# Kernel optimization log

Hardware: AMD Instinct MI355X
Metric: run time of the kernel (lower is better)

Reference implementation:

```python
import jax, jax.numpy as jnp
import numpy as np

ALPHA = 0.2  # TF leaky_relu default

def setup_inputs() -> dict:
    key = jax.random.key(0)
    ks = jax.random.split(key, 6)
    B, N, F, D = 2, 8192, 256, 128
    seq = jax.random.normal(ks[0], (B, N, F), dtype=jnp.float32)
    # Conv1D with kernel size 1 == pointwise linear
    Wf = jax.random.normal(ks[1], (F, D), dtype=jnp.float32) * (1.0 / np.sqrt(F))
    w1 = jax.random.normal(ks[2], (D, 1), dtype=jnp.float32) * (1.0 / np.sqrt(D))
    b1 = jnp.zeros((1,), dtype=jnp.float32)
    w2 = jax.random.normal(ks[3], (D, 1), dtype=jnp.float32) * (1.0 / np.sqrt(D))
    b2 = jnp.zeros((1,), dtype=jnp.float32)
    bias = jnp.zeros((D,), dtype=jnp.float32)
    return {"seq": seq, "Wf": Wf, "w1": w1, "b1": b1, "w2": w2, "b2": b2, "bias": bias}

def reference(seq, Wf, w1, b1, w2, b2, bias):
    # seq: [B,N,F] -> seq_fts: [B,N,D]
    seq_fts = jnp.einsum('bnf,fd->bnd', seq, Wf)
    f1 = jnp.einsum('bnd,do->bno', seq_fts, w1) + b1  # [B,N,1]
    f2 = jnp.einsum('bnd,do->bno', seq_fts, w2) + b2  # [B,N,1]
    logits = f1 + jnp.swapaxes(f2, 1, 2)              # [B,N,N] outer-sum
    coefs = jax.nn.softmax(jax.nn.leaky_relu(logits, ALPHA), axis=-1)
    vals = jnp.einsum('bnm,bmd->bnd', coefs, seq_fts) + bias
    return jax.nn.leaky_relu(vals, ALPHA)
```

## Files before the change

### kernel.cpp

```cpp
#include <hip/hip_runtime.h>
#include <cstddef>

#define ALPHA 0.2f
constexpr int B = 2, N = 8192, F = 256, D = 128;
constexpr int M = B * N;
constexpr int NB = 2048;
constexpr int SUB = 128;
constexpr int P = N / SUB;
constexpr int GB = 2;
constexpr int NBB = NB / GB;
constexpr int GSZ = 64;
constexpr int NGRP = NB / GSZ;
constexpr int QROWS = 8;
constexpr int DSL = 4;
constexpr int NSL = D / DSL;

#define BMIN (-10.0f)
#define BSCALE ((float)NB / 20.0f)
__device__ inline int bucket_of(float x) {
  int g = (int)((x - BMIN) * BSCALE);
  return g < 0 ? 0 : (g > NB - 1 ? NB - 1 : g);
}

__global__ __launch_bounds__(512) void k_gemm(const float* __restrict__ seq,
                                              const float* __restrict__ Wf,
                                              const float* __restrict__ w1,
                                              const float* __restrict__ b1,
                                              const float* __restrict__ w2,
                                              const float* __restrict__ b2,
                                              float* __restrict__ fts,
                                              float* __restrict__ f1,
                                              float* __restrict__ f2) {
  __shared__ float As[32][68];
  __shared__ float Bs[32][128];
  const int m0 = blockIdx.x * 64;
  const int t = threadIdx.x;
  const int colg = t & 31;
  const int rowg = t >> 5;
  float acc[4][4];
#pragma unroll
  for (int r = 0; r < 4; ++r)
#pragma unroll
    for (int c = 0; c < 4; ++c) acc[r][c] = 0.f;

  for (int kc = 0; kc < F; kc += 32) {
    {
      int row = t >> 3, k4 = t & 7;
      const float4 v = *reinterpret_cast<const float4*>(
          &seq[(size_t)(m0 + row) * F + kc + k4 * 4]);
      As[k4 * 4 + 0][row] = v.x; As[k4 * 4 + 1][row] = v.y;
      As[k4 * 4 + 2][row] = v.z; As[k4 * 4 + 3][row] = v.w;
    }
#pragma unroll
    for (int it = 0; it < 2; ++it) {
      int f = t + it * 512;
      int row = f >> 5, c4 = f & 31;
      *reinterpret_cast<float4*>(&Bs[row][c4 * 4]) =
          *reinterpret_cast<const float4*>(&Wf[(size_t)(kc + row) * D + c4 * 4]);
    }
    __syncthreads();
#pragma unroll
    for (int k = 0; k < 32; ++k) {
      const float4 a4 = *reinterpret_cast<const float4*>(&As[k][rowg * 4]);
      const float4 b4 = *reinterpret_cast<const float4*>(&Bs[k][colg * 4]);
      acc[0][0] += a4.x * b4.x; acc[0][1] += a4.x * b4.y; acc[0][2] += a4.x * b4.z; acc[0][3] += a4.x * b4.w;
      acc[1][0] += a4.y * b4.x; acc[1][1] += a4.y * b4.y; acc[1][2] += a4.y * b4.z; acc[1][3] += a4.y * b4.w;
      acc[2][0] += a4.z * b4.x; acc[2][1] += a4.z * b4.y; acc[2][2] += a4.z * b4.z; acc[2][3] += a4.z * b4.w;
      acc[3][0] += a4.w * b4.x; acc[3][1] += a4.w * b4.y; acc[3][2] += a4.w * b4.z; acc[3][3] += a4.w * b4.w;
    }
    __syncthreads();
  }
#pragma unroll
  for (int r = 0; r < 4; ++r) {
    float4 v = {acc[r][0], acc[r][1], acc[r][2], acc[r][3]};
    *reinterpret_cast<float4*>(&fts[(size_t)(m0 + rowg * 4 + r) * D + colg * 4]) = v;
  }
  const float w1v[4] = {w1[colg * 4], w1[colg * 4 + 1], w1[colg * 4 + 2], w1[colg * 4 + 3]};
  const float w2v[4] = {w2[colg * 4], w2[colg * 4 + 1], w2[colg * 4 + 2], w2[colg * 4 + 3]};
  const float b1v = b1[0], b2v = b2[0];
#pragma unroll
  for (int r = 0; r < 4; ++r) {
    float s1 = acc[r][0] * w1v[0] + acc[r][1] * w1v[1] + acc[r][2] * w1v[2] + acc[r][3] * w1v[3];
    float s2 = acc[r][0] * w2v[0] + acc[r][1] * w2v[1] + acc[r][2] * w2v[2] + acc[r][3] * w2v[3];
#pragma unroll
    for (int off = 16; off > 0; off >>= 1) {
      s1 += __shfl_down(s1, off, 32);
      s2 += __shfl_down(s2, off, 32);
    }
    if (colg == 0) {
      const int row = m0 + rowg * 4 + r;
      f1[row] = s1 + b1v;
      f2[row] = s2 + b2v;
    }
  }
}

__global__ __launch_bounds__(128) void k_hist(const float* __restrict__ f2,
                                              int* __restrict__ bid,
                                              int* __restrict__ histcnt) {
  __shared__ int hist[NB];
  const int b = blockIdx.x / P, p = blockIdx.x % P;
  const int t = threadIdx.x;
  for (int i = t; i < NB; i += 128) hist[i] = 0;
  const int j = p * SUB + t;
  float x = f2[b * N + j];
  int g = bucket_of(x);
  bid[b * N + j] = g;
  __syncthreads();
  atomicAdd(&hist[g], 1);
  __syncthreads();
  for (int i = t; i < NB; i += 128)
    histcnt[((size_t)(b * P + p)) * NB + i] = hist[i];
}

__global__ __launch_bounds__(256) void k_sub(const int* __restrict__ histcnt,
                                             int* __restrict__ substart,
                                             int* __restrict__ btot) {
  const int gid = blockIdx.x * 256 + threadIdx.x;
  const int b = gid / NB, g = gid % NB;
  int run = 0;
  for (int pp = 0; pp < P; ++pp) {
    substart[((size_t)(b * P + pp)) * NB + g] = run;
    run += histcnt[((size_t)(b * P + pp)) * NB + g];
  }
  btot[b * NB + g] = run;
}

__global__ __launch_bounds__(128) void k_scat(const float* __restrict__ f2,
                                              const int* __restrict__ bid,
                                              const int* __restrict__ substart,
                                              const int* __restrict__ btot,
                                              int* __restrict__ bstart,
                                              float* __restrict__ f2s,
                                              int* __restrict__ idxs,
                                              float* __restrict__ wps,
                                              float* __restrict__ wns) {
  __shared__ int bstart_lds[NB];
  __shared__ int bids[SUB];
  __shared__ int wsum2[2];
  const int b = blockIdx.x / P, p = blockIdx.x % P;
  const int t = threadIdx.x;
  const int lane = t & 63, wave = t >> 6;
  const size_t bN = (size_t)b * N;

  int c[16];
  int loc = 0;
#pragma unroll
  for (int i = 0; i < 16; ++i) { c[i] = btot[b * NB + t * 16 + i]; loc += c[i]; }
  int incl = loc;
#pragma unroll
  for (int off = 1; off < 64; off <<= 1) {
    int y = __shfl_up(incl, off);
    if (lane >= off) incl += y;
  }
  if (lane == 63) wsum2[wave] = incl;
  __syncthreads();
  if (wave == 1) incl += wsum2[0];
  int excl = incl - loc;
#pragma unroll
  for (int i = 0; i < 16; ++i) { bstart_lds[t * 16 + i] = excl; excl += c[i]; }
  __syncthreads();
  if (p == 0) {
    for (int i = t; i < NB; i += 128) bstart[b * (NB + 1) + i] = bstart_lds[i];
    if (t == 0) bstart[b * (NB + 1) + NB] = N;
  }

  const int j = p * SUB + t;
  const int g = bid[bN + j];
  bids[t] = g;
  __syncthreads();
  int off = bstart_lds[g] + substart[((size_t)(b * P + p)) * NB + g];
  for (int jj = 0; jj < t; ++jj) off += (bids[jj] == g);
  const float x = f2[bN + j];
  f2s[bN + off] = x;
  idxs[bN + off] = j;
  wps[bN + off] = expf(x);
  wns[bN + off] = expf(ALPHA * x);
}

__global__ __launch_bounds__(256) void k_perm(const float* __restrict__ fts,
                                              const int* __restrict__ idxs,
                                              float* __restrict__ fts_s) {
  const int tid = blockIdx.x * 256 + threadIdx.x;
  const int eg = tid >> 5;
  const int q = tid & 31;
  const int b = eg / N;
  const int j = idxs[eg];
  *reinterpret_cast<float4*>(&fts_s[(size_t)eg * D + q * 4]) =
      *reinterpret_cast<const float4*>(&fts[((size_t)b * N + j) * D + q * 4]);
}

__global__ __launch_bounds__(128) void k_bsum(const float* __restrict__ fts_s,
                                              const float* __restrict__ wps,
                                              const float* __restrict__ wns,
                                              const int* __restrict__ bstart,
                                              float* __restrict__ Wp, float* __restrict__ Wn,
                                              float* __restrict__ Cp, float* __restrict__ Cn) {
  const int b = blockIdx.x / NBB, blk = blockIdx.x % NBB;
  const int d = threadIdx.x;
  const int gbase = blk * GB;
  const size_t bN = (size_t)b * N;
  for (int gg = 0; gg < GB; ++gg) {
    const int g = gbase + gg;
    const int e0 = bstart[b * (NB + 1) + g], e1 = bstart[b * (NB + 1) + g + 1];
    float ap = 0.f, an = 0.f, sp = 0.f, sn = 0.f;
    int e = e0;
    for (; e + 4 <= e1; e += 4) {
      const float* vp = &fts_s[(bN + e) * D + d];
      const float v0 = vp[0], v1 = vp[D], v2 = vp[2 * D], v3 = vp[3 * D];
      const float p0 = wps[bN + e], p1 = wps[bN + e + 1], p2 = wps[bN + e + 2], p3 = wps[bN + e + 3];
      const float n0 = wns[bN + e], n1 = wns[bN + e + 1], n2 = wns[bN + e + 2], n3 = wns[bN + e + 3];
      ap += p0 * v0 + p1 * v1 + p2 * v2 + p3 * v3;
      an += n0 * v0 + n1 * v1 + n2 * v2 + n3 * v3;
      sp += p0 + p1 + p2 + p3;
      sn += n0 + n1 + n2 + n3;
    }
    for (; e < e1; ++e) {
      const float v = fts_s[(bN + e) * D + d];
      const float wp = wps[bN + e], wn = wns[bN + e];
      ap += wp * v; an += wn * v; sp += wp; sn += wn;
    }
    Wp[((size_t)b * NB + g) * D + d] = ap;
    Wn[((size_t)b * NB + g) * D + d] = an;
    if (d == 0) { Cp[b * NB + g] = sp; Cn[b * NB + g] = sn; }
  }
}

__global__ __launch_bounds__(128) void k_scan(const float* __restrict__ Wp, const float* __restrict__ Wn,
                                              const float* __restrict__ Cp, const float* __restrict__ Cn,
                                              float* __restrict__ BPos, float* __restrict__ BNeg,
                                              float* __restrict__ CpB, float* __restrict__ CnB) {
  __shared__ float gp[NGRP][DSL], gn[NGRP][DSL];
  __shared__ float cgp[NGRP], cgn[NGRP];
  const int b = blockIdx.x / NSL, sl = blockIdx.x % NSL;
  const int t = threadIdx.x;
  const int d4 = t & (DSL - 1), grp = t >> 2;
  const int d = sl * DSL + d4;
  const size_t base = (size_t)b * NB;

  float sp = 0.f, sn = 0.f;
  for (int gg = 0; gg < GSZ; ++gg) {
    const int g = grp * GSZ + gg;
    sp += Wp[(base + g) * D + d];
    sn += Wn[(base + g) * D + d];
  }
  gp[grp][d4] = sp; gn[grp][d4] = sn;
  if (sl == 0 && d4 == 0) {
    float cp = 0.f, cn = 0.f;
    for (int gg = 0; gg < GSZ; ++gg) { const int g = grp * GSZ + gg; cp += Cp[base + g]; cn += Cn[base + g]; }
    cgp[grp] = cp; cgn[grp] = cn;
  }
  __syncthreads();

  if (t < DSL) {
    float run = 0.f;
    for (int g2 = 0; g2 < NGRP; ++g2) { const float v = gn[g2][t]; gn[g2][t] = run; run += v; }
  } else if (t < 2 * DSL) {
    const int dd = t - DSL;
    float run = 0.f;
    for (int g2 = NGRP - 1; g2 >= 0; --g2) { const float v = gp[g2][dd]; gp[g2][dd] = run; run += v; }
  } else if (sl == 0 && t == 2 * DSL) {
    float run = 0.f;
    for (int g2 = 0; g2 < NGRP; ++g2) { const float v = cgn[g2]; cgn[g2] = run; run += v; }
  } else if (sl == 0 && t == 2 * DSL + 1) {
    float run = 0.f;
    for (int g2 = NGRP - 1; g2 >= 0; --g2) { const float v = cgp[g2]; cgp[g2] = run; run += v; }
  }
  __syncthreads();

  float runn = gn[grp][d4];
  for (int gg = 0; gg < GSZ; ++gg) {
    const int g = grp * GSZ + gg;
    BNeg[(base + g) * D + d] = runn;
    runn += Wn[(base + g) * D + d];
  }
  float runp = gp[grp][d4];
  for (int gg = GSZ - 1; gg >= 0; --gg) {
    const int g = grp * GSZ + gg;
    BPos[(base + g) * D + d] = runp;
    runp += Wp[(base + g) * D + d];
  }
  if (sl == 0 && d4 == 0) {
    float rn = cgn[grp];
    for (int gg = 0; gg < GSZ; ++gg) { const int g = grp * GSZ + gg; CnB[base + g] = rn; rn += Cn[base + g]; }
    float rp = cgp[grp];
    for (int gg = GSZ - 1; gg >= 0; --gg) { const int g = grp * GSZ + gg; CpB[base + g] = rp; rp += Cp[base + g]; }
  }
}

__global__ __launch_bounds__(256) void k_query(const float* __restrict__ f1,
                                               const float* __restrict__ f2s,
                                               const float* __restrict__ wps,
                                               const float* __restrict__ wns,
                                               const float* __restrict__ fts_s,
                                               const int* __restrict__ bstart,
                                               const float* __restrict__ BPos, const float* __restrict__ BNeg,
                                               const float* __restrict__ CpB, const float* __restrict__ CnB,
                                               const float* __restrict__ bias,
                                               float* __restrict__ out) {
  const int r = threadIdx.x >> 5;
  const int lane = threadIdx.x & 31;
  const int row = blockIdx.x * QROWS + r;
  const int b = row / N;
  const size_t bN = (size_t)b * N;
  const int d4 = lane * 4;
  const float f1v = f1[row];
  const float th = -f1v;
  const int g = bucket_of(th);
  const int base = bstart[b * (NB + 1) + g];
  const int end  = bstart[b * (NB + 1) + g + 1];
  float4 sn = *reinterpret_cast<const float4*>(&BNeg[((size_t)b * NB + g) * D + d4]);
  float4 sp = *reinterpret_cast<const float4*>(&BPos[((size_t)b * NB + g) * D + d4]);
  float cn = CnB[b * NB + g];
  float cp = CpB[b * NB + g];
  for (int e = base; e < end; ++e) {
    const float key = f2s[bN + e];
    const float wn_raw = wns[bN + e];
    const float wp_raw = wps[bN + e];
    const float4 v = *reinterpret_cast<const float4*>(&fts_s[(bN + e) * D + d4]);
    const bool neg = (key <= th);
    const float wn = neg ? wn_raw : 0.f;
    const float wp = neg ? 0.f : wp_raw;
    sn.x += wn * v.x; sn.y += wn * v.y; sn.z += wn * v.z; sn.w += wn * v.w;
    sp.x += wp * v.x; sp.y += wp * v.y; sp.z += wp * v.z; sp.w += wp * v.w;
    cn += wn; cp += wp;
  }
  const float wqp = expf(f1v), wqn = expf(ALPHA * f1v);
  const float denom = wqp * cp + wqn * cn;
  const float inv = 1.0f / denom;
  const float4 bi = *reinterpret_cast<const float4*>(&bias[d4]);
  float4 val;
  val.x = (wqp * sp.x + wqn * sn.x) * inv + bi.x;
  val.y = (wqp * sp.y + wqn * sn.y) * inv + bi.y;
  val.z = (wqp * sp.z + wqn * sn.z) * inv + bi.z;
  val.w = (wqp * sp.w + wqn * sn.w) * inv + bi.w;
  val.x = val.x >= 0.f ? val.x : ALPHA * val.x;
  val.y = val.y >= 0.f ? val.y : ALPHA * val.y;
  val.z = val.z >= 0.f ? val.z : ALPHA * val.z;
  val.w = val.w >= 0.f ? val.w : ALPHA * val.w;
  *reinterpret_cast<float4*>(&out[(size_t)row * D + d4]) = val;
}

extern "C" void kernel_launch(void* const* d_in, const int* in_sizes, int n_in,
                              void* d_out, int out_size, void* d_ws, size_t ws_size,
                              hipStream_t stream) {
  const float* seq  = (const float*)d_in[0];
  const float* Wf   = (const float*)d_in[1];
  const float* w1   = (const float*)d_in[2];
  const float* b1   = (const float*)d_in[3];
  const float* w2   = (const float*)d_in[4];
  const float* b2   = (const float*)d_in[5];
  const float* bias = (const float*)d_in[6];
  float* out = (float*)d_out;

  char* ws = (char*)d_ws;
  size_t off = 0;
  auto alloc = [&](size_t bytes) -> void* {
    void* p = ws + off;
    off = (off + bytes + 255) & ~(size_t)255;
    return p;
  };

  float* fts     = (float*)alloc((size_t)M * D * 4);
  float* fts_s   = (float*)alloc((size_t)M * D * 4);
  float* f1      = (float*)alloc((size_t)M * 4);
  float* f2      = (float*)alloc((size_t)M * 4);
  float* f2s     = (float*)alloc((size_t)M * 4);
  int*   idxs    = (int*)  alloc((size_t)M * 4);
  float* wps     = (float*)alloc((size_t)M * 4);
  float* wns     = (float*)alloc((size_t)M * 4);
  int*   bid     = (int*)  alloc((size_t)M * 4);
  int*   histcnt = (int*)  alloc((size_t)B * P * NB * 4);
  int*   substart= (int*)  alloc((size_t)B * P * NB * 4);
  int*   btot    = (int*)  alloc((size_t)B * NB * 4);
  int*   bstart  = (int*)  alloc((size_t)B * (NB + 1) * 4);
  float* Wp      = (float*)alloc((size_t)B * NB * D * 4);
  float* Wn      = (float*)alloc((size_t)B * NB * D * 4);
  float* Cp      = (float*)alloc((size_t)B * NB * 4);
  float* Cn      = (float*)alloc((size_t)B * NB * 4);
  float* BPos    = (float*)alloc((size_t)B * NB * D * 4);
  float* BNeg    = (float*)alloc((size_t)B * NB * D * 4);
  float* CpB     = (float*)alloc((size_t)B * NB * 4);
  float* CnB     = (float*)alloc((size_t)B * NB * 4);

  hipLaunchKernelGGL(k_gemm,  dim3(M / 64),          dim3(512), 0, stream, seq, Wf, w1, b1, w2, b2, fts, f1, f2);
  hipLaunchKernelGGL(k_hist,  dim3(B * P),           dim3(128), 0, stream, f2, bid, histcnt);
  hipLaunchKernelGGL(k_sub,   dim3(B * NB / 256),    dim3(256), 0, stream, histcnt, substart, btot);
  hipLaunchKernelGGL(k_scat,  dim3(B * P),           dim3(128), 0, stream, f2, bid, substart, btot, bstart,
                     f2s, idxs, wps, wns);
  hipLaunchKernelGGL(k_perm,  dim3(M * D / 4 / 256), dim3(256), 0, stream, fts, idxs, fts_s);
  hipLaunchKernelGGL(k_bsum,  dim3(B * NBB),         dim3(128), 0, stream, fts_s, wps, wns, bstart, Wp, Wn, Cp, Cn);
  hipLaunchKernelGGL(k_scan,  dim3(B * NSL),         dim3(128), 0, stream, Wp, Wn, Cp, Cn, BPos, BNeg, CpB, CnB);
  hipLaunchKernelGGL(k_query, dim3(M / QROWS),       dim3(256), 0, stream, f1, f2s, wps, wns, fts_s, bstart,
                     BPos, BNeg, CpB, CnB, bias, out);
}
```

Baseline: 96.70 us.

## Use split-bf16 MFMA for projection GEMM and widen scan groups

The fp32 SIMT projection GEMM is replaced by bf16 MFMA 16x16x32 instructions. Each operand is split into high and low bf16 halves, and three products are accumulated to stay close to fp32 accuracy. The f1/f2 reductions now go through 16-lane shuffles and a shared-memory combine across the two column-half waves. Separately, k_scan group size is halved to 32 and the block is doubled to 256 threads, giving more parallelism in the per-group scan. This adds conversion work in the tile loads, a small precision loss, and LDS bank-conflict risk from the transposed B stores.

```diff
diff --git a/kernel.cpp b/kernel.cpp
--- a/kernel.cpp
+++ b/kernel.cpp
@@ -9,17 +9,28 @@
 constexpr int P = N / SUB;
 constexpr int GB = 2;
 constexpr int NBB = NB / GB;
-constexpr int GSZ = 64;
+constexpr int GSZ = 32;
 constexpr int NGRP = NB / GSZ;
 constexpr int QROWS = 8;
 constexpr int DSL = 4;
 constexpr int NSL = D / DSL;
+
+typedef __attribute__((ext_vector_type(8))) short bf16x8;
+typedef __attribute__((ext_vector_type(4))) float f32x4;
 
 #define BMIN (-10.0f)
 #define BSCALE ((float)NB / 20.0f)
 __device__ inline int bucket_of(float x) {
   int g = (int)((x - BMIN) * BSCALE);
   return g < 0 ? 0 : (g > NB - 1 ? NB - 1 : g);
+}
+
+__device__ inline unsigned short bf16_rne(float x) {
+  unsigned u = __float_as_uint(x);
+  return (unsigned short)((u + 0x7FFFu + ((u >> 16) & 1u)) >> 16);
+}
+__device__ inline float bf16_tof(unsigned short h) {
+  return __uint_as_float(((unsigned)h) << 16);
 }
 
 __global__ __launch_bounds__(512) void k_gemm(const float* __restrict__ seq,
@@ -31,67 +42,89 @@
                                               float* __restrict__ fts,
                                               float* __restrict__ f1,
                                               float* __restrict__ f2) {
-  __shared__ float As[32][68];
-  __shared__ float Bs[32][128];
+  __shared__ unsigned short Ah[64][40], Al[64][40];
+  __shared__ unsigned short Bh[128][40], Bl[128][40];
+  __shared__ float part1[64][2], part2[64][2];
   const int m0 = blockIdx.x * 64;
   const int t = threadIdx.x;
-  const int colg = t & 31;
-  const int rowg = t >> 5;
-  float acc[4][4];
-#pragma unroll
-  for (int r = 0; r < 4; ++r)
-#pragma unroll
-    for (int c = 0; c < 4; ++c) acc[r][c] = 0.f;
+  const int w = t >> 6;
+  const int lane = t & 63;
+  const int q = lane >> 4, rt = lane & 15;
+  const int r0 = (w & 3) * 16;
+  const int c0 = (w >> 2) * 64;
+  f32x4 acc[4];
+#pragma unroll
+  for (int ct = 0; ct < 4; ++ct) acc[ct] = (f32x4){0.f, 0.f, 0.f, 0.f};
 
   for (int kc = 0; kc < F; kc += 32) {
     {
-      int row = t >> 3, k4 = t & 7;
+      const int row = t >> 3, k4 = t & 7;
       const float4 v = *reinterpret_cast<const float4*>(
           &seq[(size_t)(m0 + row) * F + kc + k4 * 4]);
-      As[k4 * 4 + 0][row] = v.x; As[k4 * 4 + 1][row] = v.y;
-      As[k4 * 4 + 2][row] = v.z; As[k4 * 4 + 3][row] = v.w;
+      const float vv[4] = {v.x, v.y, v.z, v.w};
+#pragma unroll
+      for (int i = 0; i < 4; ++i) {
+        const unsigned short h = bf16_rne(vv[i]);
+        Ah[row][k4 * 4 + i] = h;
+        Al[row][k4 * 4 + i] = bf16_rne(vv[i] - bf16_tof(h));
+      }
     }
 #pragma unroll
     for (int it = 0; it < 2; ++it) {
-      int f = t + it * 512;
-      int row = f >> 5, c4 = f & 31;
-      *reinterpret_cast<float4*>(&Bs[row][c4 * 4]) =
-          *reinterpret_cast<const float4*>(&Wf[(size_t)(kc + row) * D + c4 * 4]);
+      const int f = t + it * 512;
+      const int kr = f >> 5, c4 = f & 31;
+      const float4 v = *reinterpret_cast<const float4*>(
+          &Wf[(size_t)(kc + kr) * D + c4 * 4]);
+      const float vv[4] = {v.x, v.y, v.z, v.w};
+#pragma unroll
+      for (int i = 0; i < 4; ++i) {
+        const unsigned short h = bf16_rne(vv[i]);
+        Bh[c4 * 4 + i][kr] = h;
+        Bl[c4 * 4 + i][kr] = bf16_rne(vv[i] - bf16_tof(h));
+      }
     }
     __syncthreads();
-#pragma unroll
-    for (int k = 0; k < 32; ++k) {
-      const float4 a4 = *reinterpret_cast<const float4*>(&As[k][rowg * 4]);
-      const float4 b4 = *reinterpret_cast<const float4*>(&Bs[k][colg * 4]);
-      acc[0][0] += a4.x * b4.x; acc[0][1] += a4.x * b4.y; acc[0][2] += a4.x * b4.z; acc[0][3] += a4.x * b4.w;
-      acc[1][0] += a4.y * b4.x; acc[1][1] += a4.y * b4.y; acc[1][2] += a4.y * b4.z; acc[1][3] += a4.y * b4.w;
-      acc[2][0] += a4.z * b4.x; acc[2][1] += a4.z * b4.y; acc[2][2] += a4.z * b4.z; acc[2][3] += a4.z * b4.w;
-      acc[3][0] += a4.w * b4.x; acc[3][1] += a4.w * b4.y; acc[3][2] += a4.w * b4.z; acc[3][3] += a4.w * b4.w;
+    const bf16x8 ah = *reinterpret_cast<const bf16x8*>(&Ah[r0 + rt][q * 8]);
+    const bf16x8 al = *reinterpret_cast<const bf16x8*>(&Al[r0 + rt][q * 8]);
+#pragma unroll
+    for (int ct = 0; ct < 4; ++ct) {
+      const bf16x8 bh = *reinterpret_cast<const bf16x8*>(&Bh[c0 + ct * 16 + rt][q * 8]);
+      const bf16x8 bl = *reinterpret_cast<const bf16x8*>(&Bl[c0 + ct * 16 + rt][q * 8]);
+      acc[ct] = __builtin_amdgcn_mfma_f32_16x16x32_bf16(ah, bh, acc[ct], 0, 0, 0);
+      acc[ct] = __builtin_amdgcn_mfma_f32_16x16x32_bf16(al, bh, acc[ct], 0, 0, 0);
+      acc[ct] = __builtin_amdgcn_mfma_f32_16x16x32_bf16(ah, bl, acc[ct], 0, 0, 0);
     }
     __syncthreads();
   }
 #pragma unroll
-  for (int r = 0; r < 4; ++r) {
-    float4 v = {acc[r][0], acc[r][1], acc[r][2], acc[r][3]};
-    *reinterpret_cast<float4*>(&fts[(size_t)(m0 + rowg * 4 + r) * D + colg * 4]) = v;
-  }
-  const float w1v[4] = {w1[colg * 4], w1[colg * 4 + 1], w1[colg * 4 + 2], w1[colg * 4 + 3]};
-  const float w2v[4] = {w2[colg * 4], w2[colg * 4 + 1], w2[colg * 4 + 2], w2[colg * 4 + 3]};
-  const float b1v = b1[0], b2v = b2[0];
-#pragma unroll
-  for (int r = 0; r < 4; ++r) {
-    float s1 = acc[r][0] * w1v[0] + acc[r][1] * w1v[1] + acc[r][2] * w1v[2] + acc[r][3] * w1v[3];
-    float s2 = acc[r][0] * w2v[0] + acc[r][1] * w2v[1] + acc[r][2] * w2v[2] + acc[r][3] * w2v[3];
-#pragma unroll
-    for (int off = 16; off > 0; off >>= 1) {
-      s1 += __shfl_down(s1, off, 32);
-      s2 += __shfl_down(s2, off, 32);
-    }
-    if (colg == 0) {
-      const int row = m0 + rowg * 4 + r;
-      f1[row] = s1 + b1v;
-      f2[row] = s2 + b2v;
-    }
+  for (int ct = 0; ct < 4; ++ct)
+#pragma unroll
+    for (int reg = 0; reg < 4; ++reg)
+      fts[(size_t)(m0 + r0 + q * 4 + reg) * D + c0 + ct * 16 + rt] = acc[ct][reg];
+
+#pragma unroll
+  for (int reg = 0; reg < 4; ++reg) {
+    float s1 = 0.f, s2 = 0.f;
+#pragma unroll
+    for (int ct = 0; ct < 4; ++ct) {
+      const int c = c0 + ct * 16 + rt;
+      s1 += acc[ct][reg] * w1[c];
+      s2 += acc[ct][reg] * w2[c];
+    }
+#pragma unroll
+    for (int off = 8; off > 0; off >>= 1) {
+      s1 += __shfl_down(s1, off, 16);
+      s2 += __shfl_down(s2, off, 16);
+    }
+    if (rt == 0) {
+      part1[r0 + q * 4 + reg][w >> 2] = s1;
+      part2[r0 + q * 4 + reg][w >> 2] = s2;
+    }
+  }
+  __syncthreads();
+  if (t < 64) {
+    f1[m0 + t] = part1[t][0] + part1[t][1] + b1[0];
+    f2[m0 + t] = part2[t][0] + part2[t][1] + b2[0];
   }
 }
 
@@ -226,7 +259,7 @@
   }
 }
 
-__global__ __launch_bounds__(128) void k_scan(const float* __restrict__ Wp, const float* __restrict__ Wn,
+__global__ __launch_bounds__(256) void k_scan(const float* __restrict__ Wp, const float* __restrict__ Wn,
                                               const float* __restrict__ Cp, const float* __restrict__ Cn,
                                               float* __restrict__ BPos, float* __restrict__ BNeg,
                                               float* __restrict__ CpB, float* __restrict__ CnB) {
@@ -390,7 +423,7 @@
                      f2s, idxs, wps, wns);
   hipLaunchKernelGGL(k_perm,  dim3(M * D / 4 / 256), dim3(256), 0, stream, fts, idxs, fts_s);
   hipLaunchKernelGGL(k_bsum,  dim3(B * NBB),         dim3(128), 0, stream, fts_s, wps, wns, bstart, Wp, Wn, Cp, Cn);
-  hipLaunchKernelGGL(k_scan,  dim3(B * NSL),         dim3(128), 0, stream, Wp, Wn, Cp, Cn, BPos, BNeg, CpB, CnB);
+  hipLaunchKernelGGL(k_scan,  dim3(B * NSL),         dim3(256), 0, stream, Wp, Wn, Cp, Cn, BPos, BNeg, CpB, CnB);
   hipLaunchKernelGGL(k_query, dim3(M / QROWS),       dim3(256), 0, stream, f1, f2s, wps, wns, fts_s, bstart,
                      BPos, BNeg, CpB, CnB, bias, out);
 }
```

After: 101.1 us. +4.5%, slower.

## Double bucket count over narrower range and pack key/weights into float4

Applied to the files above, without the earlier changes.

Doubles the number of sort buckets and narrows the bucket range, so each query's boundary bucket holds fewer elements to scan linearly. The per-element key, exp(x) and exp(alpha*x) values are packed into one float4 array, so the bucket-sum and query kernels each make one vector load instead of three scalar loads. In exchange the bucket-sum, scan, histogram and prefix arrays double in size, and the scan kernel now uses 256 threads because NGRP doubled. Keys outside [-6,6] clamp into the edge buckets, which could make those buckets larger.

```diff
diff --git a/kernel.cpp b/kernel.cpp
--- a/kernel.cpp
+++ b/kernel.cpp
@@ -4,7 +4,7 @@
 #define ALPHA 0.2f
 constexpr int B = 2, N = 8192, F = 256, D = 128;
 constexpr int M = B * N;
-constexpr int NB = 2048;
+constexpr int NB = 4096;
 constexpr int SUB = 128;
 constexpr int P = N / SUB;
 constexpr int GB = 2;
@@ -14,9 +14,10 @@
 constexpr int QROWS = 8;
 constexpr int DSL = 4;
 constexpr int NSL = D / DSL;
-
-#define BMIN (-10.0f)
-#define BSCALE ((float)NB / 20.0f)
+constexpr int BPT = NB / 128;
+
+#define BMIN (-6.0f)
+#define BSCALE ((float)NB / 12.0f)
 __device__ inline int bucket_of(float x) {
   int g = (int)((x - BMIN) * BSCALE);
   return g < 0 ? 0 : (g > NB - 1 ? NB - 1 : g);
@@ -131,10 +132,8 @@
                                               const int* __restrict__ substart,
                                               const int* __restrict__ btot,
                                               int* __restrict__ bstart,
-                                              float* __restrict__ f2s,
-                                              int* __restrict__ idxs,
-                                              float* __restrict__ wps,
-                                              float* __restrict__ wns) {
+                                              float4* __restrict__ kw,
+                                              int* __restrict__ idxs) {
   __shared__ int bstart_lds[NB];
   __shared__ int bids[SUB];
   __shared__ int wsum2[2];
@@ -143,10 +142,10 @@
   const int lane = t & 63, wave = t >> 6;
   const size_t bN = (size_t)b * N;
 
-  int c[16];
+  int c[BPT];
   int loc = 0;
 #pragma unroll
-  for (int i = 0; i < 16; ++i) { c[i] = btot[b * NB + t * 16 + i]; loc += c[i]; }
+  for (int i = 0; i < BPT; ++i) { c[i] = btot[b * NB + t * BPT + i]; loc += c[i]; }
   int incl = loc;
 #pragma unroll
   for (int off = 1; off < 64; off <<= 1) {
@@ -158,7 +157,7 @@
   if (wave == 1) incl += wsum2[0];
   int excl = incl - loc;
 #pragma unroll
-  for (int i = 0; i < 16; ++i) { bstart_lds[t * 16 + i] = excl; excl += c[i]; }
+  for (int i = 0; i < BPT; ++i) { bstart_lds[t * BPT + i] = excl; excl += c[i]; }
   __syncthreads();
   if (p == 0) {
     for (int i = t; i < NB; i += 128) bstart[b * (NB + 1) + i] = bstart_lds[i];
@@ -172,10 +171,8 @@
   int off = bstart_lds[g] + substart[((size_t)(b * P + p)) * NB + g];
   for (int jj = 0; jj < t; ++jj) off += (bids[jj] == g);
   const float x = f2[bN + j];
-  f2s[bN + off] = x;
+  kw[bN + off] = make_float4(x, expf(x), expf(ALPHA * x), 0.f);
   idxs[bN + off] = j;
-  wps[bN + off] = expf(x);
-  wns[bN + off] = expf(ALPHA * x);
 }
 
 __global__ __launch_bounds__(256) void k_perm(const float* __restrict__ fts,
@@ -191,8 +188,7 @@
 }
 
 __global__ __launch_bounds__(128) void k_bsum(const float* __restrict__ fts_s,
-                                              const float* __restrict__ wps,
-                                              const float* __restrict__ wns,
+                                              const float4* __restrict__ kw,
                                               const int* __restrict__ bstart,
                                               float* __restrict__ Wp, float* __restrict__ Wn,
                                               float* __restrict__ Cp, float* __restrict__ Cn) {
@@ -208,17 +204,16 @@
     for (; e + 4 <= e1; e += 4) {
       const float* vp = &fts_s[(bN + e) * D + d];
       const float v0 = vp[0], v1 = vp[D], v2 = vp[2 * D], v3 = vp[3 * D];
-      const float p0 = wps[bN + e], p1 = wps[bN + e + 1], p2 = wps[bN + e + 2], p3 = wps[bN + e + 3];
-      const float n0 = wns[bN + e], n1 = wns[bN + e + 1], n2 = wns[bN + e + 2], n3 = wns[bN + e + 3];
-      ap += p0 * v0 + p1 * v1 + p2 * v2 + p3 * v3;
-      an += n0 * v0 + n1 * v1 + n2 * v2 + n3 * v3;
-      sp += p0 + p1 + p2 + p3;
-      sn += n0 + n1 + n2 + n3;
+      const float4 k0 = kw[bN + e], k1 = kw[bN + e + 1], k2 = kw[bN + e + 2], k3 = kw[bN + e + 3];
+      ap += k0.y * v0 + k1.y * v1 + k2.y * v2 + k3.y * v3;
+      an += k0.z * v0 + k1.z * v1 + k2.z * v2 + k3.z * v3;
+      sp += k0.y + k1.y + k2.y + k3.y;
+      sn += k0.z + k1.z + k2.z + k3.z;
     }
     for (; e < e1; ++e) {
       const float v = fts_s[(bN + e) * D + d];
-      const float wp = wps[bN + e], wn = wns[bN + e];
-      ap += wp * v; an += wn * v; sp += wp; sn += wn;
+      const float4 k0 = kw[bN + e];
+      ap += k0.y * v; an += k0.z * v; sp += k0.y; sn += k0.z;
     }
     Wp[((size_t)b * NB + g) * D + d] = ap;
     Wn[((size_t)b * NB + g) * D + d] = an;
@@ -226,7 +221,7 @@
   }
 }
 
-__global__ __launch_bounds__(128) void k_scan(const float* __restrict__ Wp, const float* __restrict__ Wn,
+__global__ __launch_bounds__(256) void k_scan(const float* __restrict__ Wp, const float* __restrict__ Wn,
                                               const float* __restrict__ Cp, const float* __restrict__ Cn,
                                               float* __restrict__ BPos, float* __restrict__ BNeg,
                                               float* __restrict__ CpB, float* __restrict__ CnB) {
@@ -289,9 +284,7 @@
 }
 
 __global__ __launch_bounds__(256) void k_query(const float* __restrict__ f1,
-                                               const float* __restrict__ f2s,
-                                               const float* __restrict__ wps,
-                                               const float* __restrict__ wns,
+                                               const float4* __restrict__ kw,
                                                const float* __restrict__ fts_s,
                                                const int* __restrict__ bstart,
                                                const float* __restrict__ BPos, const float* __restrict__ BNeg,
@@ -314,13 +307,11 @@
   float cn = CnB[b * NB + g];
   float cp = CpB[b * NB + g];
   for (int e = base; e < end; ++e) {
-    const float key = f2s[bN + e];
-    const float wn_raw = wns[bN + e];
-    const float wp_raw = wps[bN + e];
+    const float4 kwe = kw[bN + e];
     const float4 v = *reinterpret_cast<const float4*>(&fts_s[(bN + e) * D + d4]);
-    const bool neg = (key <= th);
-    const float wn = neg ? wn_raw : 0.f;
-    const float wp = neg ? 0.f : wp_raw;
+    const bool neg = (kwe.x <= th);
+    const float wn = neg ? kwe.z : 0.f;
+    const float wp = neg ? 0.f : kwe.y;
     sn.x += wn * v.x; sn.y += wn * v.y; sn.z += wn * v.z; sn.w += wn * v.w;
     sp.x += wp * v.x; sp.y += wp * v.y; sp.z += wp * v.z; sp.w += wp * v.w;
     cn += wn; cp += wp;
@@ -361,36 +352,34 @@
     return p;
   };
 
-  float* fts     = (float*)alloc((size_t)M * D * 4);
-  float* fts_s   = (float*)alloc((size_t)M * D * 4);
-  float* f1      = (float*)alloc((size_t)M * 4);
-  float* f2      = (float*)alloc((size_t)M * 4);
-  float* f2s     = (float*)alloc((size_t)M * 4);
-  int*   idxs    = (int*)  alloc((size_t)M * 4);
-  float* wps     = (float*)alloc((size_t)M * 4);
-  float* wns     = (float*)alloc((size_t)M * 4);
-  int*   bid     = (int*)  alloc((size_t)M * 4);
-  int*   histcnt = (int*)  alloc((size_t)B * P * NB * 4);
-  int*   substart= (int*)  alloc((size_t)B * P * NB * 4);
-  int*   btot    = (int*)  alloc((size_t)B * NB * 4);
-  int*   bstart  = (int*)  alloc((size_t)B * (NB + 1) * 4);
-  float* Wp      = (float*)alloc((size_t)B * NB * D * 4);
-  float* Wn      = (float*)alloc((size_t)B * NB * D * 4);
-  float* Cp      = (float*)alloc((size_t)B * NB * 4);
-  float* Cn      = (float*)alloc((size_t)B * NB * 4);
-  float* BPos    = (float*)alloc((size_t)B * NB * D * 4);
-  float* BNeg    = (float*)alloc((size_t)B * NB * D * 4);
-  float* CpB     = (float*)alloc((size_t)B * NB * 4);
-  float* CnB     = (float*)alloc((size_t)B * NB * 4);
+  float*  fts     = (float*) alloc((size_t)M * D * 4);
+  float*  fts_s   = (float*) alloc((size_t)M * D * 4);
+  float*  f1      = (float*) alloc((size_t)M * 4);
+  float*  f2      = (float*) alloc((size_t)M * 4);
+  float4* kw      = (float4*)alloc((size_t)M * 16);
+  int*    idxs    = (int*)   alloc((size_t)M * 4);
+  int*    bid     = (int*)   alloc((size_t)M * 4);
+  int*    histcnt = (int*)   alloc((size_t)B * P * NB * 4);
+  int*    substart= (int*)   alloc((size_t)B * P * NB * 4);
+  int*    btot    = (int*)   alloc((size_t)B * NB * 4);
+  int*    bstart  = (int*)   alloc((size_t)B * (NB + 1) * 4);
+  float*  Wp      = (float*) alloc((size_t)B * NB * D * 4);
+  float*  Wn      = (float*) alloc((size_t)B * NB * D * 4);
+  float*  Cp      = (float*) alloc((size_t)B * NB * 4);
+  float*  Cn      = (float*) alloc((size_t)B * NB * 4);
+  float*  BPos    = (float*) alloc((size_t)B * NB * D * 4);
+  float*  BNeg    = (float*) alloc((size_t)B * NB * D * 4);
+  float*  CpB     = (float*) alloc((size_t)B * NB * 4);
+  float*  CnB     = (float*) alloc((size_t)B * NB * 4);
 
   hipLaunchKernelGGL(k_gemm,  dim3(M / 64),          dim3(512), 0, stream, seq, Wf, w1, b1, w2, b2, fts, f1, f2);
   hipLaunchKernelGGL(k_hist,  dim3(B * P),           dim3(128), 0, stream, f2, bid, histcnt);
   hipLaunchKernelGGL(k_sub,   dim3(B * NB / 256),    dim3(256), 0, stream, histcnt, substart, btot);
   hipLaunchKernelGGL(k_scat,  dim3(B * P),           dim3(128), 0, stream, f2, bid, substart, btot, bstart,
-                     f2s, idxs, wps, wns);
+                     kw, idxs);
   hipLaunchKernelGGL(k_perm,  dim3(M * D / 4 / 256), dim3(256), 0, stream, fts, idxs, fts_s);
-  hipLaunchKernelGGL(k_bsum,  dim3(B * NBB),         dim3(128), 0, stream, fts_s, wps, wns, bstart, Wp, Wn, Cp, Cn);
-  hipLaunchKernelGGL(k_scan,  dim3(B * NSL),         dim3(128), 0, stream, Wp, Wn, Cp, Cn, BPos, BNeg, CpB, CnB);
-  hipLaunchKernelGGL(k_query, dim3(M / QROWS),       dim3(256), 0, stream, f1, f2s, wps, wns, fts_s, bstart,
+  hipLaunchKernelGGL(k_bsum,  dim3(B * NBB),         dim3(128), 0, stream, fts_s, kw, bstart, Wp, Wn, Cp, Cn);
+  hipLaunchKernelGGL(k_scan,  dim3(B * NSL),         dim3(256), 0, stream, Wp, Wn, Cp, Cn, BPos, BNeg, CpB, CnB);
+  hipLaunchKernelGGL(k_query, dim3(M / QROWS),       dim3(256), 0, stream, f1, kw, fts_s, bstart,
                      BPos, BNeg, CpB, CnB, bias, out);
 }
```

After: 101.3 us. +4.8%, slower.
